# Kernel tuning notes

Hardware: AMD Instinct MI355X
Metric: run time of the kernel (lower is better)

Reference implementation:

```python
import jax, jax.numpy as jnp
import numpy as np

VAR_NUM, IN_DIM, OUT_DIM = 3, 8, 32
N_PTS, M_PTS, K_LAST = 8192, 2048, 10
RADIUS = 0.0342
PROJ_HIDDEN = 64
N_DIM = 2
MLP_DIMS = [2 * N_DIM + OUT_DIM, 80, 80, OUT_DIM]  # [36, 80, 80, 32]


def _gelu(x):
    # torch F.gelu default = exact erf form
    return jax.nn.gelu(x, approximate=False)


def _radius_neighbors(data, queries, r):
    # CSR-style neighbor lists (indices grouped per query), chunked for memory
    idx_chunks = []
    counts = np.zeros(queries.shape[0], np.int64)
    r2 = r * r
    for s in range(0, queries.shape[0], 1024):
        q = queries[s:s + 1024]
        d2 = ((q[:, None, :] - data[None, :, :]) ** 2).sum(-1)
        mask = d2 <= r2
        _, cols = np.nonzero(mask)  # row-major -> grouped by query
        idx_chunks.append(cols.astype(np.int32))
        counts[s:s + q.shape[0]] = mask.sum(1)
    return np.concatenate(idx_chunks), counts.astype(np.int32)


def _knn(data, queries, k):
    out = np.zeros((queries.shape[0], k), np.int32)
    for s in range(0, queries.shape[0], 1024):
        q = queries[s:s + 1024]
        d2 = ((q[:, None, :] - data[None, :, :]) ** 2).sum(-1)
        out[s:s + q.shape[0]] = np.argpartition(d2, k, axis=1)[:, :k]
    return out.reshape(-1)


def _mlp_params(key, dims):
    Ws, bs = [], []
    for i in range(len(dims) - 1):
        key, k1 = jax.random.split(key)
        Ws.append(jax.random.normal(k1, (dims[i], dims[i + 1]), jnp.float32) / np.sqrt(dims[i]).astype(np.float32))
        bs.append(jnp.zeros((dims[i + 1],), jnp.float32))
    return Ws, bs


def setup_inputs():
    rng = np.random.default_rng(0)
    input_grid = rng.uniform(size=(N_PTS, N_DIM)).astype(np.float32)
    output_grid = rng.uniform(size=(M_PTS, N_DIM)).astype(np.float32)
    nbr_index, nbr_counts = _radius_neighbors(input_grid, input_grid, RADIUS)
    nbr_seg = np.repeat(np.arange(N_PTS, dtype=np.int32), nbr_counts)
    nbr_last_index = _knn(input_grid, output_grid, K_LAST)

    key = jax.random.key(0)
    ks = jax.random.split(key, 4)
    inp = jax.random.normal(ks[0], (1, N_PTS, VAR_NUM * IN_DIM), jnp.float32)
    pW, pb = _mlp_params(ks[1], [IN_DIM, PROJ_HIDDEN, OUT_DIM])
    it0_W, it0_b = _mlp_params(ks[2], MLP_DIMS)
    it1_W, it1_b = _mlp_params(ks[3], MLP_DIMS)
    return dict(
        inp=inp,
        input_grid=jnp.asarray(input_grid), output_grid=jnp.asarray(output_grid),
        proj_W0=pW[0], proj_b0=pb[0], proj_W1=pW[1], proj_b1=pb[1],
        it0_W0=it0_W[0], it0_b0=it0_b[0], it0_W1=it0_W[1], it0_b1=it0_b[1], it0_W2=it0_W[2], it0_b2=it0_b[2],
        it1_W0=it1_W[0], it1_b0=it1_b[0], it1_W1=it1_W[1], it1_b1=it1_b[1], it1_W2=it1_W[2], it1_b2=it1_b[2],
        nbr_index=jnp.asarray(nbr_index), nbr_seg=jnp.asarray(nbr_seg),
        nbr_counts=jnp.asarray(nbr_counts), nbr_last_index=jnp.asarray(nbr_last_index),
    )


def _mlp3(x, W0, b0, W1, b1, W2, b2):
    x = _gelu(x @ W0 + b0)
    x = _gelu(x @ W1 + b1)
    return x @ W2 + b2


def reference(inp, input_grid, output_grid, proj_W0, proj_b0, proj_W1, proj_b1,
              it0_W0, it0_b0, it0_W1, it0_b1, it0_W2, it0_b2,
              it1_W0, it1_b0, it1_W1, it1_b1, it1_W2, it1_b2,
              nbr_index, nbr_seg, nbr_counts, nbr_last_index):
    B, N, _ = inp.shape  # B must be 1 (module's IT indexing assumes it)
    x = inp.reshape(B * N, VAR_NUM, IN_DIM)
    # pointwise projection MLP (gelu between layers)
    x = _gelu(x @ proj_W0 + proj_b0) @ proj_W1 + proj_b1  # (N, V, OUT_DIM)

    inv_counts = (1.0 / jnp.maximum(nbr_counts, 1).astype(x.dtype))[:, None]
    y_pos = input_grid[nbr_index]        # (E, 2) neighbor positions
    self_pos = input_grid[nbr_seg]       # (E, 2) query positions
    last_y = input_grid[nbr_last_index]                    # (M*K, 2)
    last_self = jnp.repeat(output_grid, K_LAST, axis=0)    # (M*K, 2)

    outs = []
    for v in range(VAR_NUM):
        f = x[:, v, :]
        # IT layer 0: radius neighborhoods on input grid, residual add
        agg = jnp.concatenate([y_pos, self_pos, f[nbr_index]], axis=-1)  # (E, 36)
        h = _mlp3(agg, it0_W0, it0_b0, it0_W1, it0_b1, it0_W2, it0_b2)
        f = jax.ops.segment_sum(h, nbr_seg, num_segments=N) * inv_counts + f
        # IT layer 1 (last): fixed-K neighbors from input grid to output grid, mean
        agg = jnp.concatenate([last_y, last_self, f[nbr_last_index]], axis=-1)
        h = _mlp3(agg, it1_W0, it1_b0, it1_W1, it1_b1, it1_W2, it1_b2)
        outs.append(h.reshape(M_PTS, K_LAST, OUT_DIM).mean(axis=1))
    # original concatenates temp[None] along dim=2 -> (1, M, V*OUT_DIM)
    return jnp.concatenate(outs, axis=-1)[None]
```

## Files before the change

kernel.cpp:

```cpp
#include <hip/hip_runtime.h>
#include <hip/hip_bf16.h>
#include <math.h>

#define N_PTS 8192
#define M_PTS 2048
#define KLAST 10
#define VARS 3
#define OUTD 32
#define D1 80
#define D2 80
#define PB 16
#define LPTS 8
#define NT 768
#define NWAVES 12
#define TPCH 104
#define W0P 72
#define W1P 104
#define RP 40
#define W0SZ (D1 * W0P)
#define W1SZ (D1 * W1P)
#define W2SZ (OUTD * W1P)
#define WPACK (W0SZ + W1SZ + W2SZ)

typedef float f4 __attribute__((ext_vector_type(4)));
typedef short bf16x8 __attribute__((ext_vector_type(8)));

__device__ __forceinline__ float gelu_f(float x) {
    float x2 = x * x;
    float s = x * __builtin_fmaf(0.1029418f, x2, 2.3022083f);
    float u = __builtin_amdgcn_exp2f(s);
    float r = __builtin_amdgcn_rcpf(u + 1.0f);
    return __builtin_fmaf(-x, r, x);
}
__device__ __forceinline__ unsigned short f2bf(float x) {
    unsigned int u = __float_as_uint(x);
    u += 0x7FFF + ((u >> 16) & 1);
    return (unsigned short)(u >> 16);
}
__device__ __forceinline__ float bf2f(unsigned short h) {
    return __uint_as_float(((unsigned int)h) << 16);
}
__device__ __forceinline__ int pk2(float a, float b) {
    __hip_bfloat162 h = __float22bfloat162_rn(float2{a, b});
    int r; __builtin_memcpy(&r, &h, 4); return r;
}

__device__ __forceinline__ void pack_weights(
    const float* __restrict__ W0g, const float* __restrict__ W1g,
    const float* __restrict__ W2g, unsigned short* __restrict__ wp, int t)
{
    for (int idx = t; idx < W0SZ; idx += 256) {
        int col = idx / W0P, k = idx - col * W0P;
        float w = (k < 32) ? W0g[(k + 4) * D1 + col]
                           : ((k < 36) ? W0g[(k - 32) * D1 + col] : 0.0f);
        wp[idx] = f2bf(w);
    }
    for (int idx = t; idx < W1SZ; idx += 256) {
        int col = idx / W1P, k = idx - col * W1P;
        wp[W0SZ + idx] = f2bf((k < D2) ? W1g[k * D1 + col] : 0.0f);
    }
    for (int idx = t; idx < W2SZ; idx += 256) {
        int col = idx / W1P, k = idx - col * W1P;
        wp[W0SZ + W1SZ + idx] = f2bf((k < D2) ? W2g[k * OUTD + col] : 0.0f);
    }
}

__device__ __forceinline__ void stage_packed(
    unsigned short* Wall, float* bs, const unsigned short* __restrict__ wpack,
    const float* __restrict__ b0g, const float* __restrict__ b1g,
    const float* __restrict__ b2g, int t)
{
    for (int idx = t; idx < WPACK / 8; idx += NT)
        ((int4*)Wall)[idx] = ((const int4*)wpack)[idx];
    for (int idx = t; idx < 192; idx += NT)
        bs[idx] = (idx < 80) ? b0g[idx] : (idx < 160 ? b1g[idx - 80] : b2g[idx - 160]);
}

__device__ __forceinline__ void mlp_chunk(
    int4 featsi, int4 posfi, unsigned short* Trow,
    const unsigned short* W0h, const unsigned short* W1h,
    const unsigned short* W2h, const float* bs, int lm, int quad)
{
    bf16x8 b1f0 = *(bf16x8*)&featsi;
    bf16x8 b1f1 = *(bf16x8*)&posfi;
#pragma unroll 1
    for (int cb = 0; cb < 5; ++cb) {
        f4 acc = *(const f4*)&bs[cb * 16 + quad * 4];
        bf16x8 a0 = *(const bf16x8*)&W0h[(cb * 16 + lm) * W0P + quad * 8];
        bf16x8 a1 = *(const bf16x8*)&W0h[(cb * 16 + lm) * W0P + 32 + quad * 8];
        acc = __builtin_amdgcn_mfma_f32_16x16x32_bf16(a0, b1f0, acc, 0, 0, 0);
        acc = __builtin_amdgcn_mfma_f32_16x16x32_bf16(a1, b1f1, acc, 0, 0, 0);
        *(int2*)&Trow[cb * 16 + quad * 4] =
            make_int2(pk2(gelu_f(acc.x), gelu_f(acc.y)),
                      pk2(gelu_f(acc.z), gelu_f(acc.w)));
    }
    bf16x8 b2f[3];
    b2f[0] = *(const bf16x8*)&Trow[quad * 8];
    b2f[1] = *(const bf16x8*)&Trow[32 + quad * 8];
    b2f[2] = *(const bf16x8*)&Trow[64 + quad * 8];
#pragma unroll 1
    for (int cb = 0; cb < 5; ++cb) {
        f4 acc = *(const f4*)&bs[80 + cb * 16 + quad * 4];
        const unsigned short* wh = &W1h[(cb * 16 + lm) * W1P + quad * 8];
        bf16x8 h0 = *(const bf16x8*)&wh[0];
        bf16x8 h1 = *(const bf16x8*)&wh[32];
        bf16x8 h2 = *(const bf16x8*)&wh[64];
        acc = __builtin_amdgcn_mfma_f32_16x16x32_bf16(h0, b2f[0], acc, 0, 0, 0);
        acc = __builtin_amdgcn_mfma_f32_16x16x32_bf16(h1, b2f[1], acc, 0, 0, 0);
        acc = __builtin_amdgcn_mfma_f32_16x16x32_bf16(h2, b2f[2], acc, 0, 0, 0);
        *(int2*)&Trow[cb * 16 + quad * 4] =
            make_int2(pk2(gelu_f(acc.x), gelu_f(acc.y)),
                      pk2(gelu_f(acc.z), gelu_f(acc.w)));
    }
    bf16x8 b3f[3];
    b3f[0] = *(const bf16x8*)&Trow[quad * 8];
    b3f[1] = *(const bf16x8*)&Trow[32 + quad * 8];
    b3f[2] = *(const bf16x8*)&Trow[64 + quad * 8];
    float* po = (float*)Trow;
#pragma unroll 1
    for (int cb = 0; cb < 2; ++cb) {
        f4 acc = *(const f4*)&bs[160 + cb * 16 + quad * 4];
        const unsigned short* wh = &W2h[(cb * 16 + lm) * W1P + quad * 8];
        bf16x8 h0 = *(const bf16x8*)&wh[0];
        bf16x8 h1 = *(const bf16x8*)&wh[32];
        bf16x8 h2 = *(const bf16x8*)&wh[64];
        acc = __builtin_amdgcn_mfma_f32_16x16x32_bf16(h0, b3f[0], acc, 0, 0, 0);
        acc = __builtin_amdgcn_mfma_f32_16x16x32_bf16(h1, b3f[1], acc, 0, 0, 0);
        acc = __builtin_amdgcn_mfma_f32_16x16x32_bf16(h2, b3f[2], acc, 0, 0, 0);
        *(f4*)&po[cb * 16 + quad * 4] = acc;
    }
}

__global__ __launch_bounds__(256) void proj_scan_kernel(
    const float* __restrict__ inp, const float* __restrict__ grid_in,
    const float* __restrict__ W0, const float* __restrict__ b0,
    const float* __restrict__ W1, const float* __restrict__ b1,
    unsigned short* __restrict__ f0b,
    const int* __restrict__ counts, int* __restrict__ offsets,
    const float* __restrict__ i0W0, const float* __restrict__ i0W1,
    const float* __restrict__ i0W2, unsigned short* __restrict__ wpack0,
    const float* __restrict__ i1W0, const float* __restrict__ i1W1,
    const float* __restrict__ i1W2, unsigned short* __restrict__ wpack1)
{
    const int t = threadIdx.x;
    if (blockIdx.x == 769) { pack_weights(i0W0, i0W1, i0W2, wpack0, t); return; }
    if (blockIdx.x == 770) { pack_weights(i1W0, i1W1, i1W2, wpack1, t); return; }
    if (blockIdx.x == 768) {
        __shared__ int ws2[4], wx2[4];
        const int lane = t & 63, wave = t >> 6;
        int4 a[8];
#pragma unroll
        for (int i = 0; i < 8; ++i) a[i] = ((const int4*)counts)[t * 8 + i];
        int s = 0;
#pragma unroll
        for (int i = 0; i < 8; ++i) s += a[i].x + a[i].y + a[i].z + a[i].w;
        int x = s;
#pragma unroll
        for (int d = 1; d < 64; d <<= 1) {
            int y = __shfl_up(x, d);
            if (lane >= d) x += y;
        }
        if (lane == 63) ws2[wave] = x;
        __syncthreads();
        if (t == 0) {
            wx2[0] = 0;
            wx2[1] = ws2[0];
            wx2[2] = ws2[0] + ws2[1];
            wx2[3] = ws2[0] + ws2[1] + ws2[2];
        }
        __syncthreads();
        int base = wx2[wave] + (x - s);
#pragma unroll
        for (int i = 0; i < 8; ++i) {
            int4 c = a[i];
            int4 o;
            o.x = base; base += c.x;
            o.y = base; base += c.y;
            o.z = base; base += c.z;
            o.w = base; base += c.w;
            ((int4*)offsets)[t * 8 + i] = o;
        }
        return;
    }
    __shared__ float W0s[8 * 64];
    __shared__ float W1s[64 * OUTD];
    __shared__ float xs[32 * 8];
    __shared__ float H[32 * 64];
    const int r0 = blockIdx.x * 32;
    for (int idx = t; idx < 512; idx += 256) W0s[idx] = W0[idx];
    for (int idx = t; idx < 64 * OUTD; idx += 256) W1s[idx] = W1[idx];
    xs[t] = inp[r0 * 8 + t];
    if (t < 32) {
        int row = r0 + t, n = row / 3, v = row - n * 3;
        *(int*)(f0b + ((size_t)(v << 13) + n) * RP + 32) =
            pk2(grid_in[2 * n], grid_in[2 * n + 1]);
    }
    __syncthreads();
#pragma unroll 1
    for (int p = 0; p < 8; ++p) {
        int o = t + 256 * p, r = o >> 6, col = o & 63;
        float s = b0[col];
#pragma unroll
        for (int k = 0; k < 8; ++k) s += xs[r * 8 + k] * W0s[k * 64 + col];
        H[o] = gelu_f(s);
    }
    __syncthreads();
#pragma unroll 1
    for (int p = 0; p < 4; ++p) {
        int o = t + 256 * p, r = o >> 5, c = o & 31;
        float s = b1[c];
#pragma unroll 8
        for (int k = 0; k < 64; ++k) s += H[r * 64 + k] * W1s[k * OUTD + c];
        int row = r0 + r;
        int n = row / 3, v = row - n * 3;
        f0b[((size_t)(v << 13) + n) * RP + c] = f2bf(s);
    }
}

__global__ __launch_bounds__(768, 6) void agg_kernel(
    const float* __restrict__ grid_in, const unsigned short* __restrict__ f0b,
    const int* __restrict__ nbr_index, const int* __restrict__ offsets,
    const int* __restrict__ counts,
    const unsigned short* __restrict__ wpack,
    const float* __restrict__ b0g, const float* __restrict__ b1g,
    const float* __restrict__ b2g,
    unsigned short* __restrict__ f1b)
{
    __shared__ __attribute__((aligned(16))) unsigned short Tb[NWAVES * 16 * TPCH];
    __shared__ __attribute__((aligned(16))) unsigned short Wall[WPACK];
    __shared__ __attribute__((aligned(16))) float bs[192];
    __shared__ __attribute__((aligned(16))) float accH[VARS * PB * 32];
    __shared__ int offs[PB + 1];
    __shared__ int px2b[PB];
    __shared__ float invb[PB];

    const unsigned short* W0h = Wall;
    const unsigned short* W1h = Wall + W0SZ;
    const unsigned short* W2h = Wall + W0SZ + W1SZ;

    const int t = threadIdx.x;
    const int lane = t & 63, wave = t >> 6;
    const int lm = lane & 15, quad = lane >> 4;
    const int p0 = blockIdx.x * PB;

    stage_packed(Wall, bs, wpack, b0g, b1g, b2g, t);
    if (t < PB) {
        offs[t] = offsets[p0 + t];
        int c = counts[p0 + t];
        invb[t] = 1.0f / (float)(c > 1 ? c : 1);
        px2b[t] = pk2(grid_in[2 * (p0 + t)], grid_in[2 * (p0 + t) + 1]);
    }
    if (t == PB) offs[PB] = offsets[p0 + PB - 1] + counts[p0 + PB - 1];
    for (int idx = t; idx < VARS * PB * 32; idx += NT) accH[idx] = 0.0f;
    __syncthreads();

    unsigned short* TbW = Tb + (wave * 16) * TPCH;
    if (lane < 32)
        *(int4*)(TbW + (lane >> 1) * TPCH + 80 + (lane & 1) * 8) = make_int4(0, 0, 0, 0);

    const int e0 = offs[0];
    const int cntT = offs[PB] - e0;
    const int Rb = VARS * cntT;
    const int nch = (Rb + 15) >> 4;

    unsigned short* Trow = TbW + lm * TPCH;

    int pkey; int4 pfeats, pposf;
    {
        int myrow = (wave << 4) + lm;
        pkey = -1; pfeats = make_int4(0,0,0,0); pposf = make_int4(0,0,0,0);
        if (myrow < Rb) {
            int myv = (myrow >= 2 * cntT) ? 2 : ((myrow >= cntT) ? 1 : 0);
            int e = e0 + myrow - myv * cntT;
            int myj = nbr_index[e];
            int lp = 0;
#pragma unroll
            for (int l = 1; l < PB; ++l) lp += (e >= offs[l]);
            pkey = myv * PB + lp;
            const unsigned short* rec = f0b + ((size_t)(myv << 13) + myj) * RP;
            pfeats = ((const int4*)rec)[quad];
            if (quad == 0) pposf = make_int4(*(const int*)(rec + 32), px2b[lp], 0, 0);
        }
    }

    for (int ch = wave; ch < nch; ch += NWAVES) {
        int ckey = pkey; int4 cfeats = pfeats, cposf = pposf;
        int nc = ch + NWAVES;
        pkey = -1; pfeats = make_int4(0,0,0,0); pposf = make_int4(0,0,0,0);
        if (nc < nch) {
            int myrow = (nc << 4) + lm;
            if (myrow < Rb) {
                int myv = (myrow >= 2 * cntT) ? 2 : ((myrow >= cntT) ? 1 : 0);
                int e = e0 + myrow - myv * cntT;
                int myj = nbr_index[e];
                int lp = 0;
#pragma unroll
                for (int l = 1; l < PB; ++l) lp += (e >= offs[l]);
                pkey = myv * PB + lp;
                const unsigned short* rec = f0b + ((size_t)(myv << 13) + myj) * RP;
                pfeats = ((const int4*)rec)[quad];
                if (quad == 0) pposf = make_int4(*(const int*)(rec + 32), px2b[lp], 0, 0);
            }
        }
        if (ckey < 0) { cfeats = make_int4(0,0,0,0); cposf = make_int4(0,0,0,0); }
        mlp_chunk(cfeats, cposf, Trow, W0h, W1h, W2h, bs, lm, quad);
        int col = lane & 31, eo = lane >> 5;
#pragma unroll 1
        for (int e2 = eo; e2 < 16; e2 += 2) {
            int k = __shfl(ckey, e2);
            if (k >= 0)
                atomicAdd(&accH[k * 32 + col], ((const float*)(TbW + e2 * TPCH))[col]);
        }
    }
    __syncthreads();
    for (int idx = t; idx < VARS * PB * OUTD; idx += NT) {
        int key = idx >> 5, c = idx & 31;
        int v = key >> 4, lp = key & 15;
        size_t rec = ((size_t)(v << 13) + p0 + lp) * RP;
        float val = accH[key * 32 + c] * invb[lp] + bf2f(f0b[rec + c]);
        f1b[rec + c] = f2bf(val);
    }
    if (t < VARS * PB) {
        int v = t >> 4, lp = t & 15;
        *(int*)(f1b + ((size_t)(v << 13) + p0 + lp) * RP + 32) = px2b[lp];
    }
}

__global__ __launch_bounds__(768, 6) void last_kernel(
    const unsigned short* __restrict__ f1b, const float* __restrict__ grid_out,
    const int* __restrict__ nbr_last,
    const unsigned short* __restrict__ wpack,
    const float* __restrict__ b0g, const float* __restrict__ b1g,
    const float* __restrict__ b2g,
    float* __restrict__ out)
{
    __shared__ __attribute__((aligned(16))) unsigned short Tb[NWAVES * 16 * TPCH];
    __shared__ __attribute__((aligned(16))) unsigned short Wall[WPACK];
    __shared__ __attribute__((aligned(16))) float bs[192];
    __shared__ __attribute__((aligned(16))) float accH[LPTS * VARS * 32];
    __shared__ int pxo2b[LPTS];

    const unsigned short* W0h = Wall;
    const unsigned short* W1h = Wall + W0SZ;
    const unsigned short* W2h = Wall + W0SZ + W1SZ;

    const int t = threadIdx.x;
    const int lane = t & 63, wave = t >> 6;
    const int lm = lane & 15, quad = lane >> 4;
    const int m0 = blockIdx.x * LPTS;

    stage_packed(Wall, bs, wpack, b0g, b1g, b2g, t);
    if (t < LPTS)
        pxo2b[t] = pk2(grid_out[2 * (m0 + t)], grid_out[2 * (m0 + t) + 1]);
    for (int idx = t; idx < LPTS * VARS * 32; idx += NT) accH[idx] = 0.0f;
    __syncthreads();
    unsigned short* TbW = Tb + (wave * 16) * TPCH;
    if (lane < 32)
        *(int4*)(TbW + (lane >> 1) * TPCH + 80 + (lane & 1) * 8) = make_int4(0, 0, 0, 0);

    const int Rb = LPTS * VARS * KLAST;
    const int nch = (Rb + 15) >> 4;
    unsigned short* Trow = TbW + lm * TPCH;

    for (int ch = wave; ch < nch; ch += NWAVES) {
        int myrow = (ch << 4) + lm;
        int ckey = -1; int4 cfeats = make_int4(0,0,0,0), cposf = make_int4(0,0,0,0);
        if (myrow < Rb) {
            int lp = myrow / 30, rr = myrow - lp * 30;
            int v = rr / KLAST, kk = rr - v * KLAST;
            int myj = nbr_last[(m0 + lp) * KLAST + kk];
            ckey = lp * VARS + v;
            const unsigned short* rec = f1b + ((size_t)(v << 13) + myj) * RP;
            cfeats = ((const int4*)rec)[quad];
            if (quad == 0) cposf = make_int4(*(const int*)(rec + 32), pxo2b[lp], 0, 0);
        }
        mlp_chunk(cfeats, cposf, Trow, W0h, W1h, W2h, bs, lm, quad);
        int col = lane & 31, eo = lane >> 5;
#pragma unroll 1
        for (int e2 = eo; e2 < 16; e2 += 2) {
            int k = __shfl(ckey, e2);
            if (k >= 0)
                atomicAdd(&accH[k * 32 + col], ((const float*)(TbW + e2 * TPCH))[col]);
        }
    }
    __syncthreads();
    if (t < LPTS * VARS * OUTD) {
        int key = t >> 5, c = t & 31;
        int lp = key / VARS, v = key - lp * VARS;
        out[((size_t)(m0 + lp) * VARS + v) * OUTD + c] = accH[key * 32 + c] * (1.0f / KLAST);
    }
}

extern "C" void kernel_launch(void* const* d_in, const int* in_sizes, int n_in,
                              void* d_out, int out_size, void* d_ws, size_t ws_size,
                              hipStream_t stream) {
    const float* inp      = (const float*)d_in[0];
    const float* grid_in  = (const float*)d_in[1];
    const float* grid_out = (const float*)d_in[2];
    const float* pW0 = (const float*)d_in[3];
    const float* pb0 = (const float*)d_in[4];
    const float* pW1 = (const float*)d_in[5];
    const float* pb1 = (const float*)d_in[6];
    const float* i0W0 = (const float*)d_in[7];
    const float* i0b0 = (const float*)d_in[8];
    const float* i0W1 = (const float*)d_in[9];
    const float* i0b1 = (const float*)d_in[10];
    const float* i0W2 = (const float*)d_in[11];
    const float* i0b2 = (const float*)d_in[12];
    const float* i1W0 = (const float*)d_in[13];
    const float* i1b0 = (const float*)d_in[14];
    const float* i1W1 = (const float*)d_in[15];
    const float* i1b1 = (const float*)d_in[16];
    const float* i1W2 = (const float*)d_in[17];
    const float* i1b2 = (const float*)d_in[18];
    const int* nbr_index  = (const int*)d_in[19];
    const int* nbr_counts = (const int*)d_in[21];
    const int* nbr_last   = (const int*)d_in[22];

    unsigned short* f0b = (unsigned short*)d_ws;
    unsigned short* f1b = f0b + (size_t)VARS * N_PTS * RP;
    int* offsets = (int*)(f1b + (size_t)VARS * N_PTS * RP);
    unsigned short* wpack0 = (unsigned short*)(offsets + N_PTS);
    unsigned short* wpack1 = wpack0 + WPACK;

    proj_scan_kernel<<<771, 256, 0, stream>>>(inp, grid_in, pW0, pb0, pW1, pb1,
                                              f0b, nbr_counts, offsets,
                                              i0W0, i0W1, i0W2, wpack0,
                                              i1W0, i1W1, i1W2, wpack1);
    agg_kernel<<<N_PTS / PB, NT, 0, stream>>>(grid_in, f0b, nbr_index, offsets,
                                              nbr_counts, wpack0,
                                              i0b0, i0b1, i0b2, f1b);
    last_kernel<<<M_PTS / LPTS, NT, 0, stream>>>(f1b, grid_out, nbr_last, wpack1,
                                                 i1b0, i1b1, i1b2,
                                                 (float*)d_out);
}
```

Baseline: 320.6 us.

## Read MLP weights from global memory instead of LDS and shrink blocks

Removes the per-block staging of the packed bf16 MLP weights into shared memory. The MFMA A-fragments are now loaded directly from global memory, relying on L1/L2 caching. Blocks are halved (8 query points, 4 output points, 512 threads, 8 waves) with launch bounds raised to 8 blocks per CU, giving more blocks and less LDS per block. The risk is that every MFMA weight fetch now goes through the vector memory path, with higher latency than LDS reads.

```diff
diff --git a/kernel.cpp b/kernel.cpp
--- a/kernel.cpp
+++ b/kernel.cpp
@@ -9,10 +9,10 @@
 #define OUTD 32
 #define D1 80
 #define D2 80
-#define PB 16
-#define LPTS 8
-#define NT 768
-#define NWAVES 12
+#define PB 8
+#define LPTS 4
+#define NT 512
+#define NWAVES 8
 #define TPCH 104
 #define W0P 72
 #define W1P 104
@@ -65,21 +65,12 @@
     }
 }
 
-__device__ __forceinline__ void stage_packed(
-    unsigned short* Wall, float* bs, const unsigned short* __restrict__ wpack,
-    const float* __restrict__ b0g, const float* __restrict__ b1g,
-    const float* __restrict__ b2g, int t)
-{
-    for (int idx = t; idx < WPACK / 8; idx += NT)
-        ((int4*)Wall)[idx] = ((const int4*)wpack)[idx];
-    for (int idx = t; idx < 192; idx += NT)
-        bs[idx] = (idx < 80) ? b0g[idx] : (idx < 160 ? b1g[idx - 80] : b2g[idx - 160]);
-}
-
 __device__ __forceinline__ void mlp_chunk(
     int4 featsi, int4 posfi, unsigned short* Trow,
-    const unsigned short* W0h, const unsigned short* W1h,
-    const unsigned short* W2h, const float* bs, int lm, int quad)
+    const unsigned short* __restrict__ W0h,
+    const unsigned short* __restrict__ W1h,
+    const unsigned short* __restrict__ W2h,
+    const float* bs, int lm, int quad)
 {
     bf16x8 b1f0 = *(bf16x8*)&featsi;
     bf16x8 b1f1 = *(bf16x8*)&posfi;
@@ -217,7 +208,7 @@
     }
 }
 
-__global__ __launch_bounds__(768, 6) void agg_kernel(
+__global__ __launch_bounds__(512, 8) void agg_kernel(
     const float* __restrict__ grid_in, const unsigned short* __restrict__ f0b,
     const int* __restrict__ nbr_index, const int* __restrict__ offsets,
     const int* __restrict__ counts,
@@ -227,23 +218,23 @@
     unsigned short* __restrict__ f1b)
 {
     __shared__ __attribute__((aligned(16))) unsigned short Tb[NWAVES * 16 * TPCH];
-    __shared__ __attribute__((aligned(16))) unsigned short Wall[WPACK];
     __shared__ __attribute__((aligned(16))) float bs[192];
     __shared__ __attribute__((aligned(16))) float accH[VARS * PB * 32];
     __shared__ int offs[PB + 1];
     __shared__ int px2b[PB];
     __shared__ float invb[PB];
 
-    const unsigned short* W0h = Wall;
-    const unsigned short* W1h = Wall + W0SZ;
-    const unsigned short* W2h = Wall + W0SZ + W1SZ;
+    const unsigned short* W0h = wpack;
+    const unsigned short* W1h = wpack + W0SZ;
+    const unsigned short* W2h = wpack + W0SZ + W1SZ;
 
     const int t = threadIdx.x;
     const int lane = t & 63, wave = t >> 6;
     const int lm = lane & 15, quad = lane >> 4;
     const int p0 = blockIdx.x * PB;
 
-    stage_packed(Wall, bs, wpack, b0g, b1g, b2g, t);
+    for (int idx = t; idx < 192; idx += NT)
+        bs[idx] = (idx < 80) ? b0g[idx] : (idx < 160 ? b1g[idx - 80] : b2g[idx - 160]);
     if (t < PB) {
         offs[t] = offsets[p0 + t];
         int c = counts[p0 + t];
@@ -315,18 +306,18 @@
     __syncthreads();
     for (int idx = t; idx < VARS * PB * OUTD; idx += NT) {
         int key = idx >> 5, c = idx & 31;
-        int v = key >> 4, lp = key & 15;
+        int v = key >> 3, lp = key & 7;
         size_t rec = ((size_t)(v << 13) + p0 + lp) * RP;
         float val = accH[key * 32 + c] * invb[lp] + bf2f(f0b[rec + c]);
         f1b[rec + c] = f2bf(val);
     }
     if (t < VARS * PB) {
-        int v = t >> 4, lp = t & 15;
+        int v = t >> 3, lp = t & 7;
         *(int*)(f1b + ((size_t)(v << 13) + p0 + lp) * RP + 32) = px2b[lp];
     }
 }
 
-__global__ __launch_bounds__(768, 6) void last_kernel(
+__global__ __launch_bounds__(512, 8) void last_kernel(
     const unsigned short* __restrict__ f1b, const float* __restrict__ grid_out,
     const int* __restrict__ nbr_last,
     const unsigned short* __restrict__ wpack,
@@ -335,21 +326,21 @@
     float* __restrict__ out)
 {
     __shared__ __attribute__((aligned(16))) unsigned short Tb[NWAVES * 16 * TPCH];
-    __shared__ __attribute__((aligned(16))) unsigned short Wall[WPACK];
     __shared__ __attribute__((aligned(16))) float bs[192];
     __shared__ __attribute__((aligned(16))) float accH[LPTS * VARS * 32];
     __shared__ int pxo2b[LPTS];
 
-    const unsigned short* W0h = Wall;
-    const unsigned short* W1h = Wall + W0SZ;
-    const unsigned short* W2h = Wall + W0SZ + W1SZ;
+    const unsigned short* W0h = wpack;
+    const unsigned short* W1h = wpack + W0SZ;
+    const unsigned short* W2h = wpack + W0SZ + W1SZ;
 
     const int t = threadIdx.x;
     const int lane = t & 63, wave = t >> 6;
     const int lm = lane & 15, quad = lane >> 4;
     const int m0 = blockIdx.x * LPTS;
 
-    stage_packed(Wall, bs, wpack, b0g, b1g, b2g, t);
+    for (int idx = t; idx < 192; idx += NT)
+        bs[idx] = (idx < 80) ? b0g[idx] : (idx < 160 ? b1g[idx - 80] : b2g[idx - 160]);
     if (t < LPTS)
         pxo2b[t] = pk2(grid_out[2 * (m0 + t)], grid_out[2 * (m0 + t) + 1]);
     for (int idx = t; idx < LPTS * VARS * 32; idx += NT) accH[idx] = 0.0f;
```

After: 307.6 us. 1.04x faster.
